# Performance work log

Hardware: AMD Instinct MI355X
Metric: run time of the kernel (lower is better)

## Reference

```python
import jax, jax.numpy as jnp
import numpy as np

UP_TIME = 1440.0
UP_DIST = 40.0
LOC_CNT = 100000
LOC_LEN = 131072
H = 256


def setup_inputs() -> dict:
    key = jax.random.key(0)
    ks = jax.random.split(key, 12)
    stdv = 1.0 / np.sqrt(H)
    u = lambda k, shape: jax.random.uniform(k, shape, jnp.float32, -stdv, stdv)
    return {
        "td_upper": jax.random.uniform(ks[0], (LOC_LEN,), jnp.float32),
        "td_lower": jax.random.uniform(ks[1], (LOC_LEN,), jnp.float32),
        "ld_upper": jax.random.uniform(ks[2], (LOC_LEN,), jnp.float32),
        "ld_lower": jax.random.uniform(ks[3], (LOC_LEN,), jnp.float32),
        "loc": jax.random.randint(ks[4], (LOC_LEN,), 0, LOC_CNT, jnp.int32),
        "hx": jax.random.normal(ks[5], (H, 1), jnp.float32),
        "weight_ih": u(ks[6], (H, H)),
        "weight_th_upper": u(ks[7], (H, H)),
        "weight_th_lower": u(ks[8], (H, H)),
        "weight_sh_upper": u(ks[9], (H, H)),
        "weight_sh_lower": u(ks[10], (H, H)),
        "location_weight": u(ks[11], (LOC_CNT, H)),
    }


def reference(td_upper, td_lower, ld_upper, ld_lower, loc, hx,
              weight_ih, weight_th_upper, weight_th_lower,
              weight_sh_upper, weight_sh_lower, location_weight):
    tu = jnp.clip(td_upper, 0.0, UP_TIME)
    tl = jnp.clip(td_lower, 0.0, UP_TIME)
    lu = jnp.clip(ld_upper, 0.0, UP_DIST)
    ll = jnp.clip(ld_lower, 0.0, UP_DIST)

    e = location_weight[loc]  # [L, H] gathered POI embeddings
    # Ttd[i] @ e[i] = (tu[i]*W_tu@e[i] + tl[i]*W_tl@e[i]) / (tu[i]+tl[i])
    a = jnp.einsum('hk,lk->lh', weight_th_upper, e)
    b = jnp.einsum('hk,lk->lh', weight_th_lower, e)
    t = (tu[:, None] * a + tl[:, None] * b) / (tu + tl)[:, None]  # [L, H]
    # Sld[i] @ t[i]
    c = jnp.einsum('hk,lk->lh', weight_sh_upper, t)
    d = jnp.einsum('hk,lk->lh', weight_sh_lower, t)
    s = (lu[:, None] * c + ll[:, None] * d) / (lu + ll)[:, None]  # [L, H]

    loc_vec = jnp.sum(s, axis=0)[:, None]  # [H, 1]
    usr_vec = weight_ih @ hx               # [H, 1]
    return jax.nn.sigmoid(loc_vec + usr_vec)
```

## Files before the change

kernel.cpp:

```cpp
#include <hip/hip_runtime.h>
#include <math.h>

#define H 256
typedef unsigned long long u64;

__global__ __launch_bounds__(256) void strnn_scatter(
    const float* __restrict__ td_u, const float* __restrict__ td_l,
    const float* __restrict__ ld_u, const float* __restrict__ ld_l,
    const int* __restrict__ loc, u64* __restrict__ U1, u64* __restrict__ U2,
    int L)
{
    const int i = blockIdx.x * blockDim.x + threadIdx.x;
    if (i >= L) return;
    const float tu = fminf(fmaxf(td_u[i], 0.f), 1440.f);
    const float tl = fminf(fmaxf(td_l[i], 0.f), 1440.f);
    const float lu = fminf(fmaxf(ld_u[i], 0.f), 40.f);
    const float ll = fminf(fmaxf(ld_l[i], 0.f), 40.f);
    const float al = tu / (tu + tl);
    const float be = lu / (lu + ll);
    const u64 alq = (u64)(unsigned)(al * 16777216.f + 0.5f);
    const u64 beq = (u64)(unsigned)(be * 16777216.f + 0.5f);
    const u64 abq = (u64)(unsigned)(al * be * 16777216.f + 0.5f);
    const int r = loc[i];
    atomicAdd(U1 + r, (alq << 32) | beq);
    atomicAdd(U2 + r, (abq << 32) | 1ull);
}

__global__ __launch_bounds__(512, 4) void strnn_accum(
    const u64* __restrict__ U1, const u64* __restrict__ U2,
    const float* __restrict__ table, float* __restrict__ v, int R)
{
    __shared__ float s_red[8][4][H];
    const int t    = threadIdx.x;
    const int wave = t >> 6;
    const int lane = t & 63;

    float4 a0 = {0,0,0,0}, a1 = {0,0,0,0}, a2 = {0,0,0,0}, a3 = {0,0,0,0};

    const int gw     = blockIdx.x * 8 + wave;
    const int stride = gridDim.x * 8 * 8;

    for (int r0 = gw * 8; r0 < R; r0 += stride) {
        uint4 q1[4], q2[4];
        #pragma unroll
        for (int k = 0; k < 4; ++k) {
            q1[k] = *(const uint4*)(U1 + r0 + 2 * k);
            q2[k] = *(const uint4*)(U2 + r0 + 2 * k);
        }
        float4 e[8];
        #pragma unroll
        for (int u = 0; u < 8; ++u) {
            int r = r0 + u;
            r = (r < R) ? r : (R - 1);
            e[u] = *(const float4*)(table + (size_t)r * H + 4 * lane);
        }
        const float S = 5.9604644775390625e-8f;
        #pragma unroll
        for (int u = 0; u < 8; ++u) {
            const uint4 q = q1[u >> 1];
            const uint4 p = q2[u >> 1];
            const float be_s = (float)((u & 1) ? q.z : q.x) * S;
            const float al_s = (float)((u & 1) ? q.w : q.y) * S;
            const float ab   = (float)((u & 1) ? p.w : p.y) * S;
            const float n    = (float)((u & 1) ? p.z : p.x);
            const float w0 = ab;
            const float w1 = be_s - ab;
            const float w2 = al_s - ab;
            const float w3 = n - al_s - be_s + ab;
            a0.x = fmaf(w0, e[u].x, a0.x);
            a0.y = fmaf(w0, e[u].y, a0.y);
            a0.z = fmaf(w0, e[u].z, a0.z);
            a0.w = fmaf(w0, e[u].w, a0.w);
            a1.x = fmaf(w1, e[u].x, a1.x);
            a1.y = fmaf(w1, e[u].y, a1.y);
            a1.z = fmaf(w1, e[u].z, a1.z);
            a1.w = fmaf(w1, e[u].w, a1.w);
            a2.x = fmaf(w2, e[u].x, a2.x);
            a2.y = fmaf(w2, e[u].y, a2.y);
            a2.z = fmaf(w2, e[u].z, a2.z);
            a2.w = fmaf(w2, e[u].w, a2.w);
            a3.x = fmaf(w3, e[u].x, a3.x);
            a3.y = fmaf(w3, e[u].y, a3.y);
            a3.z = fmaf(w3, e[u].z, a3.z);
            a3.w = fmaf(w3, e[u].w, a3.w);
        }
    }

    *(float4*)&s_red[wave][0][4 * lane] = a0;
    *(float4*)&s_red[wave][1][4 * lane] = a1;
    *(float4*)&s_red[wave][2][4 * lane] = a2;
    *(float4*)&s_red[wave][3][4 * lane] = a3;
    __syncthreads();
    const int col = t & 255;
    #pragma unroll
    for (int cc = 0; cc < 2; ++cc) {
        const int c = (t >> 8) * 2 + cc;
        float s = 0.f;
        #pragma unroll
        for (int w_ = 0; w_ < 8; ++w_)
            s += s_red[w_][c][col];
        atomicAdd(&v[c * H + col], s);
    }
}

__global__ __launch_bounds__(256) void strnn_mid(
    const float* __restrict__ Wtu, const float* __restrict__ Wtl,
    const float* __restrict__ Wih, const float* __restrict__ hx,
    const float* __restrict__ v, float* __restrict__ pqu)
{
    const int wave = (blockIdx.x * blockDim.x + threadIdx.x) >> 6;
    const int lane = threadIdx.x & 63;
    const float* v1 = v;
    const float* v2 = v + H;
    const float* v3 = v + 2 * H;
    const float* v4 = v + 3 * H;

    float p = 0.f, q = 0.f, u = 0.f;
    #pragma unroll
    for (int i = 0; i < H; i += 64) {
        const int k = i + lane;
        const float wtu = Wtu[wave * H + k];
        const float wtl = Wtl[wave * H + k];
        p = fmaf(wtu, v1[k], fmaf(wtl, v2[k], p));
        q = fmaf(wtu, v3[k], fmaf(wtl, v4[k], q));
        u = fmaf(Wih[wave * H + k], hx[k], u);
    }
    #pragma unroll
    for (int off = 32; off > 0; off >>= 1) {
        p += __shfl_down(p, off, 64);
        q += __shfl_down(q, off, 64);
        u += __shfl_down(u, off, 64);
    }
    if (lane == 0) {
        pqu[wave]         = p;
        pqu[H + wave]     = q;
        pqu[2 * H + wave] = u;
    }
}

__global__ __launch_bounds__(256) void strnn_out(
    const float* __restrict__ Wsu, const float* __restrict__ Wsl,
    const float* __restrict__ pqu, float* __restrict__ out)
{
    const int wave = (blockIdx.x * blockDim.x + threadIdx.x) >> 6;
    const int lane = threadIdx.x & 63;
    const float* p = pqu;
    const float* q = pqu + H;
    const float* u = pqu + 2 * H;

    float s = 0.f;
    #pragma unroll
    for (int i = 0; i < H; i += 64) {
        const int k = i + lane;
        s = fmaf(Wsu[wave * H + k], p[k], fmaf(Wsl[wave * H + k], q[k], s));
    }
    #pragma unroll
    for (int off = 32; off > 0; off >>= 1)
        s += __shfl_down(s, off, 64);
    if (lane == 0)
        out[wave] = 1.f / (1.f + expf(-(s + u[wave])));
}

extern "C" void kernel_launch(void* const* d_in, const int* in_sizes, int n_in,
                              void* d_out, int out_size, void* d_ws, size_t ws_size,
                              hipStream_t stream) {
    const float* td_u  = (const float*)d_in[0];
    const float* td_l  = (const float*)d_in[1];
    const float* ld_u  = (const float*)d_in[2];
    const float* ld_l  = (const float*)d_in[3];
    const int*   loc   = (const int*)d_in[4];
    const float* hx    = (const float*)d_in[5];
    const float* Wih   = (const float*)d_in[6];
    const float* Wtu   = (const float*)d_in[7];
    const float* Wtl   = (const float*)d_in[8];
    const float* Wsu   = (const float*)d_in[9];
    const float* Wsl   = (const float*)d_in[10];
    const float* table = (const float*)d_in[11];
    const int L = in_sizes[0];
    const int R = in_sizes[11] / H;
    const int Rpad = (R + 7) & ~7;

    u64*   U1  = (u64*)d_ws;
    u64*   U2  = U1 + Rpad;
    float* v   = (float*)(U2 + Rpad);
    float* pqu = v + 4 * H;

    hipMemsetAsync(U1, 0, 2 * (size_t)Rpad * sizeof(u64) + 4 * H * sizeof(float),
                   stream);

    strnn_scatter<<<(L + 255) / 256, 256, 0, stream>>>(
        td_u, td_l, ld_u, ld_l, loc, U1, U2, L);
    strnn_accum<<<512, 512, 0, stream>>>(U1, U2, table, v, R);
    strnn_mid<<<64, 256, 0, stream>>>(Wtu, Wtl, Wih, hx, v, pqu);
    strnn_out<<<64, 256, 0, stream>>>(Wsu, Wsl, pqu, (float*)d_out);
}
```

Before: 197.4 us.

## Spread accumulator atomics over eight partial buffers and shrink accum blocks

The accumulation kernel now uses 256-thread blocks with 4 waves, each wave handling 4 rows per iteration instead of 8, launched as 1024 blocks. Block results are atomically added into one of eight partial vectors chosen by block index, which spreads contention on the same addresses. The mid kernel sums the eight partials before its matrix-vector products. This trades fewer in-flight table loads per wave and a slightly larger memset for less atomic serialization and better occupancy.

```diff
diff --git a/kernel.cpp b/kernel.cpp
--- a/kernel.cpp
+++ b/kernel.cpp
@@ -3,6 +3,7 @@
 
 #define H 256
 typedef unsigned long long u64;
+typedef unsigned u32;
 
 __global__ __launch_bounds__(256) void strnn_scatter(
     const float* __restrict__ td_u, const float* __restrict__ td_l,
@@ -26,47 +27,46 @@
     atomicAdd(U2 + r, (abq << 32) | 1ull);
 }
 
-__global__ __launch_bounds__(512, 4) void strnn_accum(
+__global__ __launch_bounds__(256) void strnn_accum(
     const u64* __restrict__ U1, const u64* __restrict__ U2,
-    const float* __restrict__ table, float* __restrict__ v, int R)
+    const float* __restrict__ table, float* __restrict__ vpart, int R)
 {
-    __shared__ float s_red[8][4][H];
+    __shared__ float s_red[4][4][H];
     const int t    = threadIdx.x;
     const int wave = t >> 6;
     const int lane = t & 63;
+    const int wid  = blockIdx.x * 4 + wave;
+    const int nw   = gridDim.x * 4;
 
     float4 a0 = {0,0,0,0}, a1 = {0,0,0,0}, a2 = {0,0,0,0}, a3 = {0,0,0,0};
+    const float S = 5.9604644775390625e-8f;
 
-    const int gw     = blockIdx.x * 8 + wave;
-    const int stride = gridDim.x * 8 * 8;
+    for (int base = wid * 4; base < R; base += nw * 4) {
+        const uint4 qa = *(const uint4*)(U1 + base);
+        const uint4 qb = *(const uint4*)(U1 + base + 2);
+        const uint4 pa = *(const uint4*)(U2 + base);
+        const uint4 pb = *(const uint4*)(U2 + base + 2);
 
-    for (int r0 = gw * 8; r0 < R; r0 += stride) {
-        uint4 q1[4], q2[4];
+        float4 e[4];
         #pragma unroll
-        for (int k = 0; k < 4; ++k) {
-            q1[k] = *(const uint4*)(U1 + r0 + 2 * k);
-            q2[k] = *(const uint4*)(U2 + r0 + 2 * k);
-        }
-        float4 e[8];
-        #pragma unroll
-        for (int u = 0; u < 8; ++u) {
-            int r = r0 + u;
+        for (int u = 0; u < 4; ++u) {
+            int r = base + u;
             r = (r < R) ? r : (R - 1);
             e[u] = *(const float4*)(table + (size_t)r * H + 4 * lane);
         }
-        const float S = 5.9604644775390625e-8f;
+
         #pragma unroll
-        for (int u = 0; u < 8; ++u) {
-            const uint4 q = q1[u >> 1];
-            const uint4 p = q2[u >> 1];
-            const float be_s = (float)((u & 1) ? q.z : q.x) * S;
-            const float al_s = (float)((u & 1) ? q.w : q.y) * S;
-            const float ab   = (float)((u & 1) ? p.w : p.y) * S;
-            const float n    = (float)((u & 1) ? p.z : p.x);
+        for (int u = 0; u < 4; ++u) {
+            const uint4 q = (u < 2) ? qa : qb;
+            const uint4 p = (u < 2) ? pa : pb;
+            const float be = (float)((u & 1) ? q.z : q.x) * S;
+            const float al = (float)((u & 1) ? q.w : q.y) * S;
+            const float ab = (float)((u & 1) ? p.w : p.y) * S;
+            const float n  = (float)((u & 1) ? p.z : p.x);
             const float w0 = ab;
-            const float w1 = be_s - ab;
-            const float w2 = al_s - ab;
-            const float w3 = n - al_s - be_s + ab;
+            const float w1 = be - ab;
+            const float w2 = al - ab;
+            const float w3 = (n - be) - w2;
             a0.x = fmaf(w0, e[u].x, a0.x);
             a0.y = fmaf(w0, e[u].y, a0.y);
             a0.z = fmaf(w0, e[u].z, a0.z);
@@ -91,38 +91,39 @@
     *(float4*)&s_red[wave][2][4 * lane] = a2;
     *(float4*)&s_red[wave][3][4 * lane] = a3;
     __syncthreads();
-    const int col = t & 255;
+    float* vp = vpart + (size_t)(blockIdx.x & 7) * 4 * H;
     #pragma unroll
-    for (int cc = 0; cc < 2; ++cc) {
-        const int c = (t >> 8) * 2 + cc;
-        float s = 0.f;
-        #pragma unroll
-        for (int w_ = 0; w_ < 8; ++w_)
-            s += s_red[w_][c][col];
-        atomicAdd(&v[c * H + col], s);
+    for (int c = 0; c < 4; ++c) {
+        float s = s_red[0][c][t] + s_red[1][c][t] + s_red[2][c][t] + s_red[3][c][t];
+        atomicAdd(&vp[c * H + t], s);
     }
 }
 
 __global__ __launch_bounds__(256) void strnn_mid(
     const float* __restrict__ Wtu, const float* __restrict__ Wtl,
     const float* __restrict__ Wih, const float* __restrict__ hx,
-    const float* __restrict__ v, float* __restrict__ pqu)
+    const float* __restrict__ vpart, float* __restrict__ pqu)
 {
     const int wave = (blockIdx.x * blockDim.x + threadIdx.x) >> 6;
     const int lane = threadIdx.x & 63;
-    const float* v1 = v;
-    const float* v2 = v + H;
-    const float* v3 = v + 2 * H;
-    const float* v4 = v + 3 * H;
 
     float p = 0.f, q = 0.f, u = 0.f;
     #pragma unroll
     for (int i = 0; i < H; i += 64) {
         const int k = i + lane;
+        float v1 = 0.f, v2 = 0.f, v3 = 0.f, v4 = 0.f;
+        #pragma unroll
+        for (int pl = 0; pl < 8; ++pl) {
+            const float* vp = vpart + (size_t)pl * 4 * H;
+            v1 += vp[k];
+            v2 += vp[H + k];
+            v3 += vp[2 * H + k];
+            v4 += vp[3 * H + k];
+        }
         const float wtu = Wtu[wave * H + k];
         const float wtl = Wtl[wave * H + k];
-        p = fmaf(wtu, v1[k], fmaf(wtl, v2[k], p));
-        q = fmaf(wtu, v3[k], fmaf(wtl, v4[k], q));
+        p = fmaf(wtu, v1, fmaf(wtl, v2, p));
+        q = fmaf(wtu, v3, fmaf(wtl, v4, q));
         u = fmaf(Wih[wave * H + k], hx[k], u);
     }
     #pragma unroll
@@ -178,19 +179,20 @@
     const float* table = (const float*)d_in[11];
     const int L = in_sizes[0];
     const int R = in_sizes[11] / H;
-    const int Rpad = (R + 7) & ~7;
+    const int Rpad = (R + 15) & ~7;
 
-    u64*   U1  = (u64*)d_ws;
-    u64*   U2  = U1 + Rpad;
-    float* v   = (float*)(U2 + Rpad);
-    float* pqu = v + 4 * H;
+    u64*   U1    = (u64*)d_ws;
+    u64*   U2    = U1 + Rpad;
+    float* vpart = (float*)(U2 + Rpad);
+    float* pqu   = vpart + 8 * 4 * H;
 
-    hipMemsetAsync(U1, 0, 2 * (size_t)Rpad * sizeof(u64) + 4 * H * sizeof(float),
+    hipMemsetAsync(U1, 0,
+                   2 * (size_t)Rpad * sizeof(u64) + 8 * 4 * H * sizeof(float),
                    stream);
 
     strnn_scatter<<<(L + 255) / 256, 256, 0, stream>>>(
         td_u, td_l, ld_u, ld_l, loc, U1, U2, L);
-    strnn_accum<<<512, 512, 0, stream>>>(U1, U2, table, v, R);
-    strnn_mid<<<64, 256, 0, stream>>>(Wtu, Wtl, Wih, hx, v, pqu);
+    strnn_accum<<<1024, 256, 0, stream>>>(U1, U2, table, vpart, R);
+    strnn_mid<<<64, 256, 0, stream>>>(Wtu, Wtl, Wih, hx, vpart, pqu);
     strnn_out<<<64, 256, 0, stream>>>(Wsu, Wsl, pqu, (float*)d_out);
 }
```

New measurement: 191.7 us. 2.9% less time.
